# Kernel optimization log

Hardware: AMD Instinct MI355X
Metric: run time of the kernel (lower is better)

The kernel has to match this reference:

```python
import jax, jax.numpy as jnp
import numpy as np

# SOM hyperparameters (match init_kwargs)
M, N_GRID = 32, 32
D = 512
BATCH = 8192
ALPHA = 0.5          # learning_rate
NUM_EPOCH_BP = 5     # hard-coded in call(): self.backprop(self.count, 5)
ITER = 0             # first call: count == 0
RADIUS_FACTOR = 1.1
GAUSSIAN_STD = 0.08
SIGMA = max(M, N_GRID) * RADIUS_FACTOR  # 35.2


def setup_inputs() -> dict:
    key = jax.random.key(0)
    k1, k2 = jax.random.split(key)
    x = jax.random.normal(k1, (BATCH, D), dtype=jnp.float32)
    som_map = jax.random.uniform(k2, (M * N_GRID, D), dtype=jnp.float32)  # RandomUniform(0,1)
    ii, jj = np.meshgrid(np.arange(M), np.arange(N_GRID), indexing='ij')
    locs = jnp.asarray(np.stack([ii.ravel(), jj.ravel()], axis=1), dtype=jnp.int32)  # [N,2]
    return {"x": x, "som_map": som_map, "locs": locs}


def reference(x, som_map, locs):
    # --- feedforward: BMU search ---
    # squared_distance[b,n] = ||x[b] - map[n]||^2, computed without the [B,N,D] blowup
    x2 = jnp.sum(x * x, axis=1, keepdims=True)                 # [B,1]
    m2 = jnp.sum(som_map * som_map, axis=1)[None, :]           # [1,N]
    sqd = x2 + m2 - 2.0 * (x @ som_map.T)                      # [B,N]
    bmu_indices = jnp.argmin(sqd, axis=1)                      # [B]
    bmu_locs = locs[bmu_indices]                               # [B,2] int

    # --- backprop (iter=0, num_epoch=5) ---
    decay = ITER * (ALPHA - 1.0) / (NUM_EPOCH_BP - 1.0)
    radius = SIGMA - decay
    alpha = ALPHA - decay

    # bmu_distance_squares[b,n] = ||locs[n] - bmu_locs[b]||^2 (grid coords)
    diff = locs[None, :, :] - bmu_locs[:, None, :]             # [B,N,2] small (int)
    bmu_d2 = jnp.sum(diff * diff, axis=2).astype(jnp.float32)  # [B,N]
    impact = jnp.exp(-bmu_d2 / (2.0 * (radius * GAUSSIAN_STD) ** 2))  # [B,N]
    lr = impact * alpha                                        # [B,N]

    # weight_update[n,d] = sum_b lr[b,n] * (x[b,d] - map[n,d])
    # = einsum('bn,bd->nd') - map * sum_b lr   (avoids the [B,N,D] intermediate)
    weight_update = jnp.einsum('bn,bd->nd', lr, x) - som_map * jnp.sum(lr, axis=0)[:, None]
    return som_map + weight_update
```

## Files before the change

### kernel.cpp

```cpp
#include <hip/hip_runtime.h>
#include <stdint.h>

#define D 512
#define KTOT 1024
#define BATCH 8192
#define NMAP 1024
#define GRID_W 32
#define ALPHA 0.5f
#define C2 15.859712f

typedef __attribute__((ext_vector_type(4))) float f32x4;
typedef __attribute__((ext_vector_type(8))) short bf16x8;
typedef __attribute__((ext_vector_type(8))) unsigned short u16x8;

static __device__ __forceinline__ unsigned short f2bf(float f) {
    uint32_t u = __float_as_uint(f);
    uint32_t r = (u + 0x7FFFu + ((u >> 16) & 1u)) >> 16;
    return (unsigned short)r;
}
static __device__ __forceinline__ float bf2f(unsigned short h) {
    return __uint_as_float(((uint32_t)h) << 16);
}

__global__ __launch_bounds__(256) void k_split_x(const float* __restrict__ x,
                                                 unsigned short* __restrict__ As,
                                                 unsigned long long* __restrict__ packed) {
    int g = blockIdx.x * 256 + threadIdx.x;
    if (g < BATCH) packed[g] = 0xFFFFFFFFFFFFFFFFull;
    int b = g >> 6;
    int k8 = (g & 63) << 3;
    const float* xp = x + (size_t)b * D + k8;
    float4 v0 = *(const float4*)xp;
    float4 v1 = *(const float4*)(xp + 4);
    float vv[8] = {v0.x, v0.y, v0.z, v0.w, v1.x, v1.y, v1.z, v1.w};
    u16x8 hi, lo;
    #pragma unroll
    for (int j = 0; j < 8; j++) {
        unsigned short h = f2bf(vv[j]);
        hi[j] = h;
        lo[j] = f2bf(vv[j] - bf2f(h));
    }
    unsigned short* row = As + (size_t)b * KTOT;
    *(u16x8*)(row + k8) = hi;
    *(u16x8*)(row + 512 + k8) = lo;
}

__global__ __launch_bounds__(256) void k_split_m(const float* __restrict__ map,
                                                 unsigned short* __restrict__ Bs,
                                                 float* __restrict__ m2) {
    int n = blockIdx.x * 4 + (threadIdx.x >> 6);
    int lane = threadIdx.x & 63;
    const float* mp = map + (size_t)n * D + lane * 8;
    float4 v0 = *(const float4*)mp;
    float4 v1 = *(const float4*)(mp + 4);
    float vv[8] = {v0.x, v0.y, v0.z, v0.w, v1.x, v1.y, v1.z, v1.w};
    u16x8 hi;
    float s = 0.f;
    #pragma unroll
    for (int j = 0; j < 8; j++) {
        s += vv[j] * vv[j];
        hi[j] = f2bf(vv[j]);
    }
    unsigned short* row = Bs + (size_t)n * KTOT;
    *(u16x8*)(row + lane * 8) = hi;
    *(u16x8*)(row + 512 + lane * 8) = hi;
    #pragma unroll
    for (int off = 32; off > 0; off >>= 1) s += __shfl_down(s, off);
    if (lane == 0) m2[n] = s;
}

#define BM 128
#define BN 128
#define BK 64

__global__ __launch_bounds__(256) void k_bmu(const unsigned short* __restrict__ As,
                                             const unsigned short* __restrict__ Bs,
                                             const float* __restrict__ m2,
                                             unsigned long long* __restrict__ packed) {
    __shared__ unsigned short Al[BM * BK];
    __shared__ unsigned short Bl[BN * BK];
    const int b0 = blockIdx.x * BM;
    const int n0 = blockIdx.y * BN;
    const int t = threadIdx.x;
    const int w = t >> 6, l = t & 63;
    const int wm = w >> 1, wn = w & 1;

    f32x4 acc[4][4];
    #pragma unroll
    for (int i = 0; i < 4; i++)
        #pragma unroll
        for (int j = 0; j < 4; j++) acc[i][j] = (f32x4)(0.f);

    const int srow = l >> 3;
    const int sslot = (l & 7) ^ (l >> 3);
    const unsigned short* agp0 = As + (size_t)(b0 + w * 32 + srow) * KTOT + sslot * 8;
    const unsigned short* bgp0 = Bs + (size_t)(n0 + w * 32 + srow) * KTOT + sslot * 8;

    for (int kt = 0; kt < KTOT; kt += BK) {
        #pragma unroll
        for (int i = 0; i < 4; i++) {
            __builtin_amdgcn_global_load_lds(
                (const __attribute__((address_space(1))) void*)(agp0 + (size_t)i * 8 * KTOT + kt),
                (__attribute__((address_space(3))) void*)(Al + w * 2048 + i * 512), 16, 0, 0);
            __builtin_amdgcn_global_load_lds(
                (const __attribute__((address_space(1))) void*)(bgp0 + (size_t)i * 8 * KTOT + kt),
                (__attribute__((address_space(3))) void*)(Bl + w * 2048 + i * 512), 16, 0, 0);
        }
        __syncthreads();

        #pragma unroll
        for (int kk = 0; kk < 2; kk++) {
            bf16x8 af[4], bfr[4];
            #pragma unroll
            for (int mi = 0; mi < 4; mi++) {
                int r = wm * 64 + mi * 16 + (l & 15);
                int slot = kk * 4 + (l >> 4);
                af[mi] = *(const bf16x8*)&Al[r * 64 + ((slot ^ (r & 7)) << 3)];
            }
            #pragma unroll
            for (int nj = 0; nj < 4; nj++) {
                int r = wn * 64 + nj * 16 + (l & 15);
                int slot = kk * 4 + (l >> 4);
                bfr[nj] = *(const bf16x8*)&Bl[r * 64 + ((slot ^ (r & 7)) << 3)];
            }
            #pragma unroll
            for (int mi = 0; mi < 4; mi++)
                #pragma unroll
                for (int nj = 0; nj < 4; nj++)
                    acc[mi][nj] = __builtin_amdgcn_mfma_f32_16x16x32_bf16(
                        af[mi], bfr[nj], acc[mi][nj], 0, 0, 0);
        }
        __syncthreads();
    }

    float m2v[4];
    #pragma unroll
    for (int nj = 0; nj < 4; nj++)
        m2v[nj] = m2[n0 + wn * 64 + nj * 16 + (l & 15)];

    #pragma unroll
    for (int mi = 0; mi < 4; mi++) {
        #pragma unroll
        for (int reg = 0; reg < 4; reg++) {
            float best = m2v[0] - 2.0f * acc[mi][0][reg];
            int bi = n0 + wn * 64 + (l & 15);
            #pragma unroll
            for (int nj = 1; nj < 4; nj++) {
                float v = m2v[nj] - 2.0f * acc[mi][nj][reg];
                int n = n0 + wn * 64 + nj * 16 + (l & 15);
                if (v < best) { best = v; bi = n; }
            }
            #pragma unroll
            for (int msk = 1; msk <= 8; msk <<= 1) {
                float ov = __shfl_xor(best, msk);
                int oi = __shfl_xor(bi, msk);
                if (ov < best || (ov == best && oi < bi)) { best = ov; bi = oi; }
            }
            if ((l & 15) == 0) {
                unsigned int fb = __float_as_uint(best);
                fb = (fb & 0x80000000u) ? ~fb : (fb | 0x80000000u);
                unsigned long long key =
                    ((unsigned long long)fb << 32) | (unsigned int)bi;
                int row = b0 + wm * 64 + mi * 16 + (l >> 4) * 4 + reg;
                atomicMin(&packed[row], key);
            }
        }
    }
}

__global__ __launch_bounds__(256) void k_scatter(const float* __restrict__ x,
                                                 const unsigned long long* __restrict__ packed,
                                                 float* __restrict__ S,
                                                 int* __restrict__ cnt) {
    __shared__ int list[BATCH];
    __shared__ int cnts[256];
    __shared__ int offs[256];
    int g = blockIdx.x;
    int t = threadIdx.x;
    int b0 = t * (BATCH / 256);

    int mybmu[BATCH / 256];
    int c = 0;
    #pragma unroll
    for (int i = 0; i < BATCH / 256; i++) {
        mybmu[i] = (int)(packed[b0 + i] & 0xFFFFFFFFull);
        c += (mybmu[i] == g) ? 1 : 0;
    }
    cnts[t] = c;
    offs[t] = c;
    __syncthreads();
    #pragma unroll
    for (int s = 1; s < 256; s <<= 1) {
        int v = (t >= s) ? offs[t - s] : 0;
        __syncthreads();
        offs[t] += v;
        __syncthreads();
    }
    int off = offs[t] - cnts[t];
    #pragma unroll
    for (int i = 0; i < BATCH / 256; i++) {
        if (mybmu[i] == g) list[off++] = b0 + i;
    }
    __syncthreads();
    int len = offs[255];

    float acc0 = 0.f, acc1 = 0.f;
    for (int i = 0; i < len; i++) {
        const float* xr = x + (size_t)list[i] * D;
        acc0 += xr[t];
        acc1 += xr[t + 256];
    }
    S[(size_t)g * D + t] = acc0;
    S[(size_t)g * D + t + 256] = acc1;
    if (t == 0) cnt[g] = len;
}

__global__ __launch_bounds__(256) void k_conv1(const float* __restrict__ S,
                                               float* __restrict__ V,
                                               const int* __restrict__ cnt,
                                               float* __restrict__ sum_lr) {
    __shared__ float tbl[GRID_W];
    __shared__ float vc[GRID_W][GRID_W];
    int gi = blockIdx.x;
    int d = blockIdx.y * 256 + threadIdx.x;
    if (threadIdx.x < GRID_W)
        tbl[threadIdx.x] = __expf(-(float)(threadIdx.x * threadIdx.x) / C2);
    __syncthreads();
    float acc[GRID_W];
    #pragma unroll
    for (int nj = 0; nj < GRID_W; nj++) acc[nj] = 0.f;
    for (int gj = 0; gj < GRID_W; gj++) {
        float s = S[(size_t)(gi * GRID_W + gj) * D + d];
        #pragma unroll
        for (int nj = 0; nj < GRID_W; nj++) {
            int dd = nj - gj; dd = dd < 0 ? -dd : dd;
            acc[nj] += tbl[dd] * s;
        }
    }
    #pragma unroll
    for (int nj = 0; nj < GRID_W; nj++)
        V[(size_t)(gi * GRID_W + nj) * D + d] = acc[nj];

    if (blockIdx.x == 0 && blockIdx.y == 0) {
        int t = threadIdx.x;
        #pragma unroll
        for (int j = 0; j < 4; j++) {
            int idx = t * 4 + j;
            int a = idx >> 5, b = idx & 31;
            float s = 0.f;
            for (int gj = 0; gj < GRID_W; gj++) {
                int dd = gj - b; dd = dd < 0 ? -dd : dd;
                s += tbl[dd] * (float)cnt[a * GRID_W + gj];
            }
            vc[a][b] = s;
        }
        __syncthreads();
        #pragma unroll
        for (int j = 0; j < 4; j++) {
            int idx = t * 4 + j;
            int a = idx >> 5, b = idx & 31;
            float s2 = 0.f;
            for (int gg = 0; gg < GRID_W; gg++) {
                int dd = gg - a; dd = dd < 0 ? -dd : dd;
                s2 += tbl[dd] * vc[gg][b];
            }
            sum_lr[idx] = ALPHA * s2;
        }
    }
}

__global__ __launch_bounds__(256) void k_conv2(const float* __restrict__ V,
                                               const float* __restrict__ map,
                                               const float* __restrict__ sum_lr,
                                               float* __restrict__ out) {
    __shared__ float tbl[GRID_W];
    int nj = blockIdx.x;
    int d = blockIdx.y * 256 + threadIdx.x;
    if (threadIdx.x < GRID_W)
        tbl[threadIdx.x] = __expf(-(float)(threadIdx.x * threadIdx.x) / C2);
    __syncthreads();
    float acc[GRID_W];
    #pragma unroll
    for (int ni = 0; ni < GRID_W; ni++) acc[ni] = 0.f;
    for (int gi = 0; gi < GRID_W; gi++) {
        float v = V[(size_t)(gi * GRID_W + nj) * D + d];
        #pragma unroll
        for (int ni = 0; ni < GRID_W; ni++) {
            int dd = ni - gi; dd = dd < 0 ? -dd : dd;
            acc[ni] += tbl[dd] * v;
        }
    }
    #pragma unroll
    for (int ni = 0; ni < GRID_W; ni++) {
        int n = ni * GRID_W + nj;
        out[(size_t)n * D + d] =
            map[(size_t)n * D + d] * (1.0f - sum_lr[n]) + ALPHA * acc[ni];
    }
}

extern "C" void kernel_launch(void* const* d_in, const int* in_sizes, int n_in,
                              void* d_out, int out_size, void* d_ws, size_t ws_size,
                              hipStream_t stream) {
    (void)in_sizes; (void)n_in; (void)out_size; (void)ws_size;
    const float* x = (const float*)d_in[0];
    const float* map = (const float*)d_in[1];
    float* out = (float*)d_out;

    char* ws = (char*)d_ws;
    unsigned long long* packed = (unsigned long long*)(ws);
    float* m2 = (float*)(ws + 65536);
    int* cnt = (int*)(ws + 69632);
    float* sum_lr = (float*)(ws + 73728);
    float* S = (float*)(ws + 77824);
    float* V = (float*)(ws + 2175, 0 );
    V = (float*)(ws + 2174976);
    unsigned short* As = (unsigned short*)(ws + 4272128);
    unsigned short* Bs = (unsigned short*)(ws + 21049344);

    k_split_x<<<BATCH * (D / 8) / 256, 256, 0, stream>>>(x, As, packed);
    k_split_m<<<NMAP / 4, 256, 0, stream>>>(map, Bs, m2);
    k_bmu<<<dim3(BATCH / BM, NMAP / BN), 256, 0, stream>>>(As, Bs, m2, packed);
    k_scatter<<<NMAP, 256, 0, stream>>>(x, packed, S, cnt);
    k_conv1<<<dim3(GRID_W, D / 256), 256, 0, stream>>>(S, V, cnt, sum_lr);
    k_conv2<<<dim3(GRID_W, D / 256), 256, 0, stream>>>(V, map, sum_lr, out);
}
```

Before: 99.43 us.

## Fuse prep and conv kernels, remap BMU grid for XCD locality

Merges the x and map bf16 split kernels into one launch, and fuses the two separable Gaussian convolution passes into a single kernel. The fused kernel recomputes the row pass per column block, so the V intermediate and its global round-trip go away. The BMU GEMM launch becomes a 1D grid with a remapped block index so neighbouring tiles land on the same XCD for L2 reuse. In exchange, the post kernel now does redundant S reads and FMAs: each of its 64 blocks rereads all 32 rows of S and redoes the horizontal convolution, so that phase does about 32x more work than before.

```diff
diff --git a/kernel.cpp b/kernel.cpp
--- a/kernel.cpp
+++ b/kernel.cpp
@@ -22,51 +22,54 @@
     return __uint_as_float(((uint32_t)h) << 16);
 }
 
-__global__ __launch_bounds__(256) void k_split_x(const float* __restrict__ x,
-                                                 unsigned short* __restrict__ As,
-                                                 unsigned long long* __restrict__ packed) {
-    int g = blockIdx.x * 256 + threadIdx.x;
-    if (g < BATCH) packed[g] = 0xFFFFFFFFFFFFFFFFull;
-    int b = g >> 6;
-    int k8 = (g & 63) << 3;
-    const float* xp = x + (size_t)b * D + k8;
-    float4 v0 = *(const float4*)xp;
-    float4 v1 = *(const float4*)(xp + 4);
-    float vv[8] = {v0.x, v0.y, v0.z, v0.w, v1.x, v1.y, v1.z, v1.w};
-    u16x8 hi, lo;
-    #pragma unroll
-    for (int j = 0; j < 8; j++) {
-        unsigned short h = f2bf(vv[j]);
-        hi[j] = h;
-        lo[j] = f2bf(vv[j] - bf2f(h));
-    }
-    unsigned short* row = As + (size_t)b * KTOT;
-    *(u16x8*)(row + k8) = hi;
-    *(u16x8*)(row + 512 + k8) = lo;
-}
-
-__global__ __launch_bounds__(256) void k_split_m(const float* __restrict__ map,
-                                                 unsigned short* __restrict__ Bs,
-                                                 float* __restrict__ m2) {
-    int n = blockIdx.x * 4 + (threadIdx.x >> 6);
-    int lane = threadIdx.x & 63;
-    const float* mp = map + (size_t)n * D + lane * 8;
-    float4 v0 = *(const float4*)mp;
-    float4 v1 = *(const float4*)(mp + 4);
-    float vv[8] = {v0.x, v0.y, v0.z, v0.w, v1.x, v1.y, v1.z, v1.w};
-    u16x8 hi;
-    float s = 0.f;
-    #pragma unroll
-    for (int j = 0; j < 8; j++) {
-        s += vv[j] * vv[j];
-        hi[j] = f2bf(vv[j]);
-    }
-    unsigned short* row = Bs + (size_t)n * KTOT;
-    *(u16x8*)(row + lane * 8) = hi;
-    *(u16x8*)(row + 512 + lane * 8) = hi;
-    #pragma unroll
-    for (int off = 32; off > 0; off >>= 1) s += __shfl_down(s, off);
-    if (lane == 0) m2[n] = s;
+__global__ __launch_bounds__(256) void k_prep(const float* __restrict__ x,
+                                              const float* __restrict__ map,
+                                              unsigned short* __restrict__ As,
+                                              unsigned short* __restrict__ Bs,
+                                              float* __restrict__ m2,
+                                              unsigned long long* __restrict__ packed) {
+    int bid = blockIdx.x;
+    if (bid < BATCH * (D / 8) / 256) {
+        int g = bid * 256 + threadIdx.x;
+        if (g < BATCH) packed[g] = 0xFFFFFFFFFFFFFFFFull;
+        int b = g >> 6;
+        int k8 = (g & 63) << 3;
+        const float* xp = x + (size_t)b * D + k8;
+        float4 v0 = *(const float4*)xp;
+        float4 v1 = *(const float4*)(xp + 4);
+        float vv[8] = {v0.x, v0.y, v0.z, v0.w, v1.x, v1.y, v1.z, v1.w};
+        u16x8 hi, lo;
+        #pragma unroll
+        for (int j = 0; j < 8; j++) {
+            unsigned short h = f2bf(vv[j]);
+            hi[j] = h;
+            lo[j] = f2bf(vv[j] - bf2f(h));
+        }
+        unsigned short* row = As + (size_t)b * KTOT;
+        *(u16x8*)(row + k8) = hi;
+        *(u16x8*)(row + 512 + k8) = lo;
+    } else {
+        int mb = bid - BATCH * (D / 8) / 256;
+        int n = mb * 4 + (threadIdx.x >> 6);
+        int lane = threadIdx.x & 63;
+        const float* mp = map + (size_t)n * D + lane * 8;
+        float4 v0 = *(const float4*)mp;
+        float4 v1 = *(const float4*)(mp + 4);
+        float vv[8] = {v0.x, v0.y, v0.z, v0.w, v1.x, v1.y, v1.z, v1.w};
+        u16x8 hi;
+        float s = 0.f;
+        #pragma unroll
+        for (int j = 0; j < 8; j++) {
+            s += vv[j] * vv[j];
+            hi[j] = f2bf(vv[j]);
+        }
+        unsigned short* row = Bs + (size_t)n * KTOT;
+        *(u16x8*)(row + lane * 8) = hi;
+        *(u16x8*)(row + 512 + lane * 8) = hi;
+        #pragma unroll
+        for (int off = 32; off > 0; off >>= 1) s += __shfl_down(s, off);
+        if (lane == 0) m2[n] = s;
+    }
 }
 
 #define BM 128
@@ -79,8 +82,9 @@
                                              unsigned long long* __restrict__ packed) {
     __shared__ unsigned short Al[BM * BK];
     __shared__ unsigned short Bl[BN * BK];
-    const int b0 = blockIdx.x * BM;
-    const int n0 = blockIdx.y * BN;
+    int wg = (blockIdx.x & 7) * 64 + (blockIdx.x >> 3);
+    const int b0 = (wg & 63) * BM;
+    const int n0 = (wg >> 6) * BN;
     const int t = threadIdx.x;
     const int w = t >> 6, l = t & 63;
     const int wm = w >> 1, wn = w & 1;
@@ -215,86 +219,58 @@
     if (t == 0) cnt[g] = len;
 }
 
-__global__ __launch_bounds__(256) void k_conv1(const float* __restrict__ S,
-                                               float* __restrict__ V,
-                                               const int* __restrict__ cnt,
-                                               float* __restrict__ sum_lr) {
+__global__ __launch_bounds__(256) void k_post(const float* __restrict__ S,
+                                              const int* __restrict__ cnt,
+                                              const float* __restrict__ map,
+                                              float* __restrict__ out) {
     __shared__ float tbl[GRID_W];
-    __shared__ float vc[GRID_W][GRID_W];
-    int gi = blockIdx.x;
-    int d = blockIdx.y * 256 + threadIdx.x;
-    if (threadIdx.x < GRID_W)
-        tbl[threadIdx.x] = __expf(-(float)(threadIdx.x * threadIdx.x) / C2);
-    __syncthreads();
-    float acc[GRID_W];
-    #pragma unroll
-    for (int nj = 0; nj < GRID_W; nj++) acc[nj] = 0.f;
-    for (int gj = 0; gj < GRID_W; gj++) {
-        float s = S[(size_t)(gi * GRID_W + gj) * D + d];
-        #pragma unroll
-        for (int nj = 0; nj < GRID_W; nj++) {
-            int dd = nj - gj; dd = dd < 0 ? -dd : dd;
-            acc[nj] += tbl[dd] * s;
-        }
-    }
-    #pragma unroll
-    for (int nj = 0; nj < GRID_W; nj++)
-        V[(size_t)(gi * GRID_W + nj) * D + d] = acc[nj];
-
-    if (blockIdx.x == 0 && blockIdx.y == 0) {
-        int t = threadIdx.x;
-        #pragma unroll
-        for (int j = 0; j < 4; j++) {
-            int idx = t * 4 + j;
-            int a = idx >> 5, b = idx & 31;
-            float s = 0.f;
-            for (int gj = 0; gj < GRID_W; gj++) {
-                int dd = gj - b; dd = dd < 0 ? -dd : dd;
-                s += tbl[dd] * (float)cnt[a * GRID_W + gj];
-            }
-            vc[a][b] = s;
-        }
-        __syncthreads();
-        #pragma unroll
-        for (int j = 0; j < 4; j++) {
-            int idx = t * 4 + j;
-            int a = idx >> 5, b = idx & 31;
-            float s2 = 0.f;
-            for (int gg = 0; gg < GRID_W; gg++) {
-                int dd = gg - a; dd = dd < 0 ? -dd : dd;
-                s2 += tbl[dd] * vc[gg][b];
-            }
-            sum_lr[idx] = ALPHA * s2;
-        }
-    }
-}
-
-__global__ __launch_bounds__(256) void k_conv2(const float* __restrict__ V,
-                                               const float* __restrict__ map,
-                                               const float* __restrict__ sum_lr,
-                                               float* __restrict__ out) {
-    __shared__ float tbl[GRID_W];
+    __shared__ float vc[GRID_W];
+    __shared__ float slr[GRID_W];
     int nj = blockIdx.x;
     int d = blockIdx.y * 256 + threadIdx.x;
-    if (threadIdx.x < GRID_W)
-        tbl[threadIdx.x] = __expf(-(float)(threadIdx.x * threadIdx.x) / C2);
-    __syncthreads();
-    float acc[GRID_W];
-    #pragma unroll
-    for (int ni = 0; ni < GRID_W; ni++) acc[ni] = 0.f;
+    int t = threadIdx.x;
+    if (t < GRID_W) tbl[t] = __expf(-(float)(t * t) / C2);
+    __syncthreads();
+    if (t < GRID_W) {
+        float s = 0.f;
+        for (int gj = 0; gj < GRID_W; gj++) {
+            int dd = gj - nj; dd = dd < 0 ? -dd : dd;
+            s += tbl[dd] * (float)cnt[t * GRID_W + gj];
+        }
+        vc[t] = s;
+    }
+    __syncthreads();
+    if (t < GRID_W) {
+        float s2 = 0.f;
+        for (int gi = 0; gi < GRID_W; gi++) {
+            int dd = gi - t; dd = dd < 0 ? -dd : dd;
+            s2 += tbl[dd] * vc[gi];
+        }
+        slr[t] = ALPHA * s2;
+    }
+    __syncthreads();
+
+    float T[GRID_W];
+    #pragma unroll
     for (int gi = 0; gi < GRID_W; gi++) {
-        float v = V[(size_t)(gi * GRID_W + nj) * D + d];
-        #pragma unroll
-        for (int ni = 0; ni < GRID_W; ni++) {
+        float s = 0.f;
+        for (int gj = 0; gj < GRID_W; gj++) {
+            int dd = nj - gj; dd = dd < 0 ? -dd : dd;
+            s += tbl[dd] * S[(size_t)(gi * GRID_W + gj) * D + d];
+        }
+        T[gi] = s;
+    }
+    #pragma unroll
+    for (int ni = 0; ni < GRID_W; ni++) {
+        float u = 0.f;
+        #pragma unroll
+        for (int gi = 0; gi < GRID_W; gi++) {
             int dd = ni - gi; dd = dd < 0 ? -dd : dd;
-            acc[ni] += tbl[dd] * v;
-        }
-    }
-    #pragma unroll
-    for (int ni = 0; ni < GRID_W; ni++) {
+            u += tbl[dd] * T[gi];
+        }
         int n = ni * GRID_W + nj;
         out[(size_t)n * D + d] =
-            map[(size_t)n * D + d] * (1.0f - sum_lr[n]) + ALPHA * acc[ni];
+            map[(size_t)n * D + d] * (1.0f - slr[ni]) + ALPHA * u;
     }
 }
 
@@ -310,17 +286,12 @@
     unsigned long long* packed = (unsigned long long*)(ws);
     float* m2 = (float*)(ws + 65536);
     int* cnt = (int*)(ws + 69632);
-    float* sum_lr = (float*)(ws + 73728);
-    float* S = (float*)(ws + 77824);
-    float* V = (float*)(ws + 2175, 0 );
-    V = (float*)(ws + 2174976);
-    unsigned short* As = (unsigned short*)(ws + 4272128);
-    unsigned short* Bs = (unsigned short*)(ws + 21049344);
-
-    k_split_x<<<BATCH * (D / 8) / 256, 256, 0, stream>>>(x, As, packed);
-    k_split_m<<<NMAP / 4, 256, 0, stream>>>(map, Bs, m2);
-    k_bmu<<<dim3(BATCH / BM, NMAP / BN), 256, 0, stream>>>(As, Bs, m2, packed);
+    float* S = (float*)(ws + 73728);
+    unsigned short* As = (unsigned short*)(ws + 2170880);
+    unsigned short* Bs = (unsigned short*)(ws + 2170880 + 16777216);
+
+    k_prep<<<BATCH * (D / 8) / 256 + NMAP / 4, 256, 0, stream>>>(x, map, As, Bs, m2, packed);
+    k_bmu<<<(BATCH / BM) * (NMAP / BN), 256, 0, stream>>>(As, Bs, m2, packed);
     k_scatter<<<NMAP, 256, 0, stream>>>(x, packed, S, cnt);
-    k_conv1<<<dim3(GRID_W, D / 256), 256, 0, stream>>>(S, V, cnt, sum_lr);
-    k_conv2<<<dim3(GRID_W, D / 256), 256, 0, stream>>>(V, map, sum_lr, out);
-}
+    k_post<<<dim3(GRID_W, D / 256), 256, 0, stream>>>(S, cnt, map, out);
+}
```

Measured after the change: 257.4 us. 159% more time.
